# Kernel tuning notes

Hardware: AMD Instinct MI355X
Metric: run time of the kernel (lower is better)

## Reference

```python
import jax, jax.numpy as jnp
import numpy as np

B, T, H, K = 64, 512, 768, 11
START_ID, END_ID = 9, 10  # tag_to_ix['<CLS>'], tag_to_ix['<SEP>']
NEG = -10000.0


def setup_inputs() -> dict:
    key = jax.random.key(0)
    k1, k2, k3, k4 = jax.random.split(key, 4)
    embeds = jax.random.normal(k1, (B, T, H), dtype=jnp.float32)
    W_fc = jax.random.normal(k2, (K, H), dtype=jnp.float32) * 0.02
    b_fc = jax.random.normal(k3, (K,), dtype=jnp.float32) * 0.02
    transitions = jax.random.normal(k4, (K, K), dtype=jnp.float32)
    # __init__ masking: no transition out of anything into START row, none into END col
    transitions = transitions.at[START_ID, :].set(NEG)
    transitions = transitions.at[:, END_ID].set(NEG)
    return {"embeds": embeds, "W_fc": W_fc, "b_fc": b_fc, "transitions": transitions}


def reference(embeds, W_fc, b_fc, transitions):
    # fc projection: feats[b,t,k] (PLM_crf path: encoder output -> Linear)
    feats = jnp.einsum('bth,kh->btk', embeds, W_fc) + b_fc  # [B,T,K]
    Bv, Tv, Kv = feats.shape

    # Viterbi: log_delta init -10000 except start tag; NOTE the original never
    # adds feats[:, 0] (loop starts at t=1), so we faithfully skip it too.
    log_delta0 = jnp.full((Bv, Kv), NEG, dtype=feats.dtype).at[:, START_ID].set(0.0)

    def step(log_delta, feat_t):
        # transitions[i, j]: score of moving from prev tag j to tag i
        scores = transitions[None, :, :] + log_delta[:, None, :]  # [B,K,K]
        psi_t = jnp.argmax(scores, axis=-1)                       # [B,K] best prev tag
        log_delta_new = jnp.max(scores, axis=-1) + feat_t         # [B,K]
        return log_delta_new, psi_t

    feats_seq = jnp.swapaxes(feats[:, 1:], 0, 1)                  # [T-1,B,K]
    log_delta, psi = jax.lax.scan(step, log_delta0, feats_seq)    # psi: [T-1,B,K]

    score = jnp.max(log_delta, axis=-1)                           # [B]
    last_tag = jnp.argmax(log_delta, axis=-1)                     # [B]

    # Backtrack: path[t] = psi[t+1][path[t+1]] for t = T-2 .. 0
    def back(next_tag, psi_t):
        tag = jnp.take_along_axis(psi_t, next_tag[:, None], axis=-1)[:, 0]
        return tag, tag

    _, path_rest = jax.lax.scan(back, last_tag, psi, reverse=True)  # [T-1,B]
    path = jnp.concatenate([jnp.swapaxes(path_rest, 0, 1), last_tag[:, None]], axis=1)  # [B,T]
    return score, path
```

## Files before the change

### kernel.cpp

```cpp
#include <hip/hip_runtime.h>

#define BB 64
#define TT 512
#define HH 768
#define KK 11
#define START_ID 9
#define NEGV -10000.0f
#define ROR1 0x121

typedef float vf2 __attribute__((ext_vector_type(2)));

__device__ __forceinline__ float ror1f(float x) {
    return __int_as_float(__builtin_amdgcn_update_dpp(0, __float_as_int(x), ROR1, 0xF, 0xF, false));
}
__device__ __forceinline__ int ror1i(int x) {
    return __builtin_amdgcn_update_dpp(0, x, ROR1, 0xF, 0xF, false);
}

__device__ __forceinline__ float rlane(float v, int l) {
    return __int_as_float(__builtin_amdgcn_readlane(__float_as_int(v), l));
}

template <int CTRL>
__device__ __forceinline__ float dpp_add(float x) {
    int yi = __builtin_amdgcn_update_dpp(0, __float_as_int(x), CTRL, 0xF, 0xF, false);
    return x + __int_as_float(yi);
}
__device__ __forceinline__ float wave_sum_to_lane63(float x) {
    x = dpp_add<0x111>(x);
    x = dpp_add<0x112>(x);
    x = dpp_add<0x114>(x);
    x = dpp_add<0x118>(x);
    x = dpp_add<0x142>(x);
    x = dpp_add<0x143>(x);
    return x;
}

__global__ __launch_bounds__(256) void fc_kernel(const float* __restrict__ embeds,
                                                 const float* __restrict__ W,
                                                 const float* __restrict__ bias,
                                                 float* __restrict__ feats) {
    const int lane = threadIdx.x & 63;
    const int wave_id = (blockIdx.x * blockDim.x + threadIdx.x) >> 6;

    float4 wf[KK][3];
#pragma unroll
    for (int k = 0; k < KK; ++k)
#pragma unroll
        for (int r = 0; r < 3; ++r)
            wf[k][r] = *reinterpret_cast<const float4*>(W + k * HH + r * 256 + lane * 4);

    float bk[KK];
#pragma unroll
    for (int k = 0; k < KK; ++k) bk[k] = bias[k];

    const int base = wave_id * 8;
#pragma unroll 1
    for (int rr = 0; rr < 8; rr += 2) {
        const float* ea = embeds + (size_t)(base + rr) * HH;
        const float* eb = ea + HH;
        float4 a0 = *reinterpret_cast<const float4*>(ea + 0   + lane * 4);
        float4 a1 = *reinterpret_cast<const float4*>(ea + 256 + lane * 4);
        float4 a2 = *reinterpret_cast<const float4*>(ea + 512 + lane * 4);
        float4 b0 = *reinterpret_cast<const float4*>(eb + 0   + lane * 4);
        float4 b1 = *reinterpret_cast<const float4*>(eb + 256 + lane * 4);
        float4 b2 = *reinterpret_cast<const float4*>(eb + 512 + lane * 4);

        vf2 va[6] = {{a0.x, a0.y}, {a0.z, a0.w}, {a1.x, a1.y},
                     {a1.z, a1.w}, {a2.x, a2.y}, {a2.z, a2.w}};
        vf2 vb[6] = {{b0.x, b0.y}, {b0.z, b0.w}, {b1.x, b1.y},
                     {b1.z, b1.w}, {b2.x, b2.y}, {b2.z, b2.w}};

        float rA[KK], rB[KK];
#pragma unroll
        for (int k = 0; k < KK; ++k) {
            vf2 wv0 = {wf[k][0].x, wf[k][0].y}, wv1 = {wf[k][0].z, wf[k][0].w};
            vf2 wv2 = {wf[k][1].x, wf[k][1].y}, wv3 = {wf[k][1].z, wf[k][1].w};
            vf2 wv4 = {wf[k][2].x, wf[k][2].y}, wv5 = {wf[k][2].z, wf[k][2].w};
            vf2 sA = va[0] * wv0;
            vf2 sB = vb[0] * wv0;
            sA += va[1] * wv1;  sB += vb[1] * wv1;
            sA += va[2] * wv2;  sB += vb[2] * wv2;
            sA += va[3] * wv3;  sB += vb[3] * wv3;
            sA += va[4] * wv4;  sB += vb[4] * wv4;
            sA += va[5] * wv5;  sB += vb[5] * wv5;
            rA[k] = wave_sum_to_lane63(sA.x + sA.y);
            rB[k] = wave_sum_to_lane63(sB.x + sB.y);
        }
        if (lane == 63) {
            float* oA = feats + (size_t)(base + rr) * KK;
#pragma unroll
            for (int k = 0; k < KK; ++k) oA[k] = rA[k] + bk[k];
#pragma unroll
            for (int k = 0; k < KK; ++k) oA[KK + k] = rB[k] + bk[k];
        }
    }
}

__global__ __launch_bounds__(256) void viterbi_kernel(const float* __restrict__ feats,
                                                      const float* __restrict__ trans,
                                                      float* __restrict__ out) {
    __shared__ __align__(16) float feats_lds[(TT + 4) * KK];
    __shared__ __align__(16) float dh[(TT - 1) * 12];
    __shared__ int psi_lds[(TT - 1) * KK];
    __shared__ float tr_lds[KK * KK];
    __shared__ int comp[15 * KK];
    __shared__ int bt[16];
    __shared__ int sh_last;

    const int tid = threadIdx.x;
    const int b = blockIdx.x;

    {
        const float4* src = reinterpret_cast<const float4*>(feats + (size_t)b * TT * KK);
        float4* dst = reinterpret_cast<float4*>(feats_lds);
        for (int i = tid; i < TT * KK / 4; i += 256) dst[i] = src[i];
        if (tid < KK * KK) tr_lds[tid] = trans[tid];
    }
    __syncthreads();

    if (tid < 64) {
        const int i = tid & 15;
        const int g = tid >> 4;
        const bool real = (i < KK);
        const int ci = real ? i : 0;

        int jr[16];
        {
            int jx = i;
#pragma unroll
            for (int r = 0; r < 16; ++r) { jr[r] = jx; jx = ror1i(jx); }
        }
        float trr[16];
#pragma unroll
        for (int r = 0; r < 16; ++r)
            trr[r] = (real && jr[r] < KK) ? tr_lds[i * KK + jr[r]] : NEGV;

        float delta = (i == START_ID) ? 0.0f : NEGV;

        auto vstep = [&](int t, float fcur) {
            if (g == 0 && real) dh[(t - 1) * 12 + i] = delta;
            float cur = delta;
            float acc = trr[0] + cur;
#pragma unroll
            for (int r = 1; r < 16; ++r) {
                cur = ror1f(cur);
                acc = fmaxf(acc, trr[r] + cur);
            }
            delta = acc + fcur;
        };

        float fr0 = feats_lds[1 * KK + ci];
        float fr1 = feats_lds[2 * KK + ci];
        float fr2 = feats_lds[3 * KK + ci];
        float fr3 = feats_lds[4 * KK + ci];

        int t = 1;
#pragma unroll 1
        for (; t <= TT - 4; t += 4) {
            vstep(t,     fr0); fr0 = feats_lds[(t + 4) * KK + ci];
            vstep(t + 1, fr1); fr1 = feats_lds[(t + 5) * KK + ci];
            vstep(t + 2, fr2); fr2 = feats_lds[(t + 6) * KK + ci];
            vstep(t + 3, fr3); fr3 = feats_lds[(t + 7) * KK + ci];
        }
        vstep(TT - 3, fr0);
        vstep(TT - 2, fr1);
        vstep(TT - 1, fr2);

        float dfin[KK];
#pragma unroll
        for (int j = 0; j < KK; ++j) dfin[j] = rlane(delta, j);
        float best = dfin[0];
        int last = 0;
#pragma unroll
        for (int j = 1; j < KK; ++j) {
            bool c = dfin[j] > best;
            best = c ? dfin[j] : best;
            last = c ? j : last;
        }
        if (tid == 0) {
            out[b] = best;
            out[BB + (size_t)b * TT + (TT - 1)] = (float)last;
            sh_last = last;
        }
    }
    __syncthreads();

    {
        const int i = tid & 15;
        const int sg = tid >> 4;
        if (i < KK) {
            float tri[KK];
#pragma unroll
            for (int j = 0; j < KK; ++j) tri[j] = tr_lds[i * KK + j];
            for (int s = sg; s < TT - 1; s += 16) {
                const float4* dr = reinterpret_cast<const float4*>(dh + s * 12);
                float4 a = dr[0], c4 = dr[1], d4 = dr[2];
                float sc[KK] = {tri[0] + a.x,  tri[1] + a.y,  tri[2] + a.z,  tri[3] + a.w,
                                tri[4] + c4.x, tri[5] + c4.y, tri[6] + c4.z, tri[7] + c4.w,
                                tri[8] + d4.x, tri[9] + d4.y, tri[10] + d4.z};
                float bv = sc[0];
                int bj = 0;
#pragma unroll
                for (int j = 1; j < KK; ++j) {
                    bool c = sc[j] > bv;
                    bv = c ? sc[j] : bv;
                    bj = c ? j : bj;
                }
                psi_lds[s * KK + i] = bj;
            }
        }
    }
    __syncthreads();

    {
        const int c = tid >> 4;
        const int i = tid & 15;
        if (c < 15 && i < KK) {
            int cur = i;
            for (int s = c * 32 + 31; s >= c * 32; --s) cur = psi_lds[s * KK + cur];
            comp[c * KK + i] = cur;
        } else if (c == 15 && i == 0) {
            int cur = sh_last;
            float* po = out + BB + (size_t)b * TT;
            for (int s = TT - 2; s >= 480; --s) {
                cur = psi_lds[s * KK + cur];
                po[s] = (float)cur;
            }
            bt[15] = cur;
        }
    }
    __syncthreads();

    if (tid == 0) {
        for (int c = 14; c >= 1; --c) bt[c] = comp[c * KK + bt[c + 1]];
    }
    __syncthreads();

    if (tid < 15) {
        const int c = tid;
        int cur = bt[c + 1];
        float* po = out + BB + (size_t)b * TT;
        for (int s = c * 32 + 31; s >= c * 32; --s) {
            cur = psi_lds[s * KK + cur];
            po[s] = (float)cur;
        }
    }
}

extern "C" void kernel_launch(void* const* d_in, const int* in_sizes, int n_in,
                              void* d_out, int out_size, void* d_ws, size_t ws_size,
                              hipStream_t stream) {
    const float* embeds = (const float*)d_in[0];
    const float* W_fc   = (const float*)d_in[1];
    const float* b_fc   = (const float*)d_in[2];
    const float* trans  = (const float*)d_in[3];
    float* out = (float*)d_out;
    float* feats = (float*)d_ws;

    fc_kernel<<<1024, 256, 0, stream>>>(embeds, W_fc, b_fc, feats);
    viterbi_kernel<<<BB, 256, 0, stream>>>(feats, trans, out);
}
```

Before: 240.0 us.

## Process two sequences per block using readlane broadcasts in Viterbi recurrence

The Viterbi kernel now handles two batch sequences per block, with each 16-lane group of the wave tracking a different sequence. The DPP rotate-based max over previous tags is replaced by broadcasting each previous delta with readlane and doing a tree max. The intent is to halve the block count and shorten the dependency chain through the max. The cost is many scalar readlane operations per step and backtracking both sequences one after the other in each block.

```diff
diff --git a/kernel.cpp b/kernel.cpp
--- a/kernel.cpp
+++ b/kernel.cpp
@@ -6,16 +6,8 @@
 #define KK 11
 #define START_ID 9
 #define NEGV -10000.0f
-#define ROR1 0x121
 
 typedef float vf2 __attribute__((ext_vector_type(2)));
-
-__device__ __forceinline__ float ror1f(float x) {
-    return __int_as_float(__builtin_amdgcn_update_dpp(0, __float_as_int(x), ROR1, 0xF, 0xF, false));
-}
-__device__ __forceinline__ int ror1i(int x) {
-    return __builtin_amdgcn_update_dpp(0, x, ROR1, 0xF, 0xF, false);
-}
 
 __device__ __forceinline__ float rlane(float v, int l) {
     return __int_as_float(__builtin_amdgcn_readlane(__float_as_int(v), l));
@@ -100,93 +92,118 @@
 __global__ __launch_bounds__(256) void viterbi_kernel(const float* __restrict__ feats,
                                                       const float* __restrict__ trans,
                                                       float* __restrict__ out) {
-    __shared__ __align__(16) float feats_lds[(TT + 4) * KK];
-    __shared__ __align__(16) float dh[(TT - 1) * 12];
-    __shared__ int psi_lds[(TT - 1) * KK];
+    __shared__ __align__(16) float feats_lds[2][(TT + 4) * KK];
+    __shared__ __align__(16) float dh[2][(TT - 1) * 12];
+    __shared__ int psi_lds[2][(TT - 1) * KK];
     __shared__ float tr_lds[KK * KK];
     __shared__ int comp[15 * KK];
-    __shared__ int bt[16];
-    __shared__ int sh_last;
+    __shared__ int btb[16];
+    __shared__ int sh_last[2];
 
     const int tid = threadIdx.x;
-    const int b = blockIdx.x;
+    const int b0 = blockIdx.x * 2;
 
     {
-        const float4* src = reinterpret_cast<const float4*>(feats + (size_t)b * TT * KK);
-        float4* dst = reinterpret_cast<float4*>(feats_lds);
-        for (int i = tid; i < TT * KK / 4; i += 256) dst[i] = src[i];
+        const float4* s0 = reinterpret_cast<const float4*>(feats + (size_t)b0 * TT * KK);
+        const float4* s1 = reinterpret_cast<const float4*>(feats + (size_t)(b0 + 1) * TT * KK);
+        float4* d0 = reinterpret_cast<float4*>(&feats_lds[0][0]);
+        float4* d1 = reinterpret_cast<float4*>(&feats_lds[1][0]);
+        for (int i = tid; i < TT * KK / 4; i += 256) { d0[i] = s0[i]; d1[i] = s1[i]; }
         if (tid < KK * KK) tr_lds[tid] = trans[tid];
     }
     __syncthreads();
 
     if (tid < 64) {
-        const int i = tid & 15;
-        const int g = tid >> 4;
+        const int lane = tid;
+        const int i = lane & 15;
+        const int q = (lane >> 4) & 1;
         const bool real = (i < KK);
         const int ci = real ? i : 0;
 
-        int jr[16];
-        {
-            int jx = i;
-#pragma unroll
-            for (int r = 0; r < 16; ++r) { jr[r] = jx; jx = ror1i(jx); }
-        }
-        float trr[16];
-#pragma unroll
-        for (int r = 0; r < 16; ++r)
-            trr[r] = (real && jr[r] < KK) ? tr_lds[i * KK + jr[r]] : NEGV;
-
+        float trr[KK];
+#pragma unroll
+        for (int j = 0; j < KK; ++j) trr[j] = real ? tr_lds[i * KK + j] : NEGV;
+
+        const float* fl = &feats_lds[q][0];
         float delta = (i == START_ID) ? 0.0f : NEGV;
 
         auto vstep = [&](int t, float fcur) {
-            if (g == 0 && real) dh[(t - 1) * 12 + i] = delta;
-            float cur = delta;
-            float acc = trr[0] + cur;
-#pragma unroll
-            for (int r = 1; r < 16; ++r) {
-                cur = ror1f(cur);
-                acc = fmaxf(acc, trr[r] + cur);
-            }
-            delta = acc + fcur;
+            if (lane < 32 && real) dh[q][(t - 1) * 12 + i] = delta;
+            float djA[KK], djB[KK];
+#pragma unroll
+            for (int j = 0; j < KK; ++j) {
+                djA[j] = rlane(delta, j);
+                djB[j] = rlane(delta, 16 + j);
+            }
+            float sA[KK], sB[KK];
+#pragma unroll
+            for (int j = 0; j < KK; ++j) { sA[j] = trr[j] + djA[j]; sB[j] = trr[j] + djB[j]; }
+            float a0 = fmaxf(fmaxf(sA[0], sA[1]), sA[2]);
+            float a1 = fmaxf(fmaxf(sA[3], sA[4]), sA[5]);
+            float a2 = fmaxf(fmaxf(sA[6], sA[7]), sA[8]);
+            float a3 = fmaxf(sA[9], sA[10]);
+            float bestA = fmaxf(fmaxf(fmaxf(a0, a1), a2), a3);
+            float c0 = fmaxf(fmaxf(sB[0], sB[1]), sB[2]);
+            float c1 = fmaxf(fmaxf(sB[3], sB[4]), sB[5]);
+            float c2 = fmaxf(fmaxf(sB[6], sB[7]), sB[8]);
+            float c3 = fmaxf(sB[9], sB[10]);
+            float bestB = fmaxf(fmaxf(fmaxf(c0, c1), c2), c3);
+            float best = q ? bestB : bestA;
+            delta = best + fcur;
         };
 
-        float fr0 = feats_lds[1 * KK + ci];
-        float fr1 = feats_lds[2 * KK + ci];
-        float fr2 = feats_lds[3 * KK + ci];
-        float fr3 = feats_lds[4 * KK + ci];
+        float fr0 = fl[1 * KK + ci];
+        float fr1 = fl[2 * KK + ci];
+        float fr2 = fl[3 * KK + ci];
+        float fr3 = fl[4 * KK + ci];
 
         int t = 1;
 #pragma unroll 1
         for (; t <= TT - 4; t += 4) {
-            vstep(t,     fr0); fr0 = feats_lds[(t + 4) * KK + ci];
-            vstep(t + 1, fr1); fr1 = feats_lds[(t + 5) * KK + ci];
-            vstep(t + 2, fr2); fr2 = feats_lds[(t + 6) * KK + ci];
-            vstep(t + 3, fr3); fr3 = feats_lds[(t + 7) * KK + ci];
+            vstep(t,     fr0); fr0 = fl[(t + 4) * KK + ci];
+            vstep(t + 1, fr1); fr1 = fl[(t + 5) * KK + ci];
+            vstep(t + 2, fr2); fr2 = fl[(t + 6) * KK + ci];
+            vstep(t + 3, fr3); fr3 = fl[(t + 7) * KK + ci];
         }
         vstep(TT - 3, fr0);
         vstep(TT - 2, fr1);
         vstep(TT - 1, fr2);
 
-        float dfin[KK];
-#pragma unroll
-        for (int j = 0; j < KK; ++j) dfin[j] = rlane(delta, j);
-        float best = dfin[0];
-        int last = 0;
-#pragma unroll
-        for (int j = 1; j < KK; ++j) {
-            bool c = dfin[j] > best;
-            best = c ? dfin[j] : best;
-            last = c ? j : last;
+        float dfA[KK], dfB[KK];
+#pragma unroll
+        for (int j = 0; j < KK; ++j) {
+            dfA[j] = rlane(delta, j);
+            dfB[j] = rlane(delta, 16 + j);
         }
         if (tid == 0) {
-            out[b] = best;
-            out[BB + (size_t)b * TT + (TT - 1)] = (float)last;
-            sh_last = last;
+            float best = dfA[0]; int last = 0;
+#pragma unroll
+            for (int j = 1; j < KK; ++j) {
+                bool c = dfA[j] > best;
+                best = c ? dfA[j] : best;
+                last = c ? j : last;
+            }
+            out[b0] = best;
+            out[BB + (size_t)b0 * TT + (TT - 1)] = (float)last;
+            sh_last[0] = last;
+        }
+        if (tid == 1) {
+            float best = dfB[0]; int last = 0;
+#pragma unroll
+            for (int j = 1; j < KK; ++j) {
+                bool c = dfB[j] > best;
+                best = c ? dfB[j] : best;
+                last = c ? j : last;
+            }
+            out[b0 + 1] = best;
+            out[BB + (size_t)(b0 + 1) * TT + (TT - 1)] = (float)last;
+            sh_last[1] = last;
         }
     }
     __syncthreads();
 
-    {
+#pragma unroll 1
+    for (int q = 0; q < 2; ++q) {
         const int i = tid & 15;
         const int sg = tid >> 4;
         if (i < KK) {
@@ -194,7 +211,7 @@
 #pragma unroll
             for (int j = 0; j < KK; ++j) tri[j] = tr_lds[i * KK + j];
             for (int s = sg; s < TT - 1; s += 16) {
-                const float4* dr = reinterpret_cast<const float4*>(dh + s * 12);
+                const float4* dr = reinterpret_cast<const float4*>(&dh[q][s * 12]);
                 float4 a = dr[0], c4 = dr[1], d4 = dr[2];
                 float sc[KK] = {tri[0] + a.x,  tri[1] + a.y,  tri[2] + a.z,  tri[3] + a.w,
                                 tri[4] + c4.x, tri[5] + c4.y, tri[6] + c4.z, tri[7] + c4.w,
@@ -207,44 +224,48 @@
                     bv = c ? sc[j] : bv;
                     bj = c ? j : bj;
                 }
-                psi_lds[s * KK + i] = bj;
+                psi_lds[q][s * KK + i] = bj;
             }
         }
     }
     __syncthreads();
 
-    {
-        const int c = tid >> 4;
-        const int i = tid & 15;
-        if (c < 15 && i < KK) {
-            int cur = i;
-            for (int s = c * 32 + 31; s >= c * 32; --s) cur = psi_lds[s * KK + cur];
-            comp[c * KK + i] = cur;
-        } else if (c == 15 && i == 0) {
-            int cur = sh_last;
-            float* po = out + BB + (size_t)b * TT;
-            for (int s = TT - 2; s >= 480; --s) {
-                cur = psi_lds[s * KK + cur];
+#pragma unroll 1
+    for (int q = 0; q < 2; ++q) {
+        {
+            const int c = tid >> 4;
+            const int i = tid & 15;
+            if (c < 15 && i < KK) {
+                int cur = i;
+                for (int s = c * 32 + 31; s >= c * 32; --s) cur = psi_lds[q][s * KK + cur];
+                comp[c * KK + i] = cur;
+            } else if (c == 15 && i == 0) {
+                int cur = sh_last[q];
+                float* po = out + BB + (size_t)(b0 + q) * TT;
+                for (int s = TT - 2; s >= 480; --s) {
+                    cur = psi_lds[q][s * KK + cur];
+                    po[s] = (float)cur;
+                }
+                btb[15] = cur;
+            }
+        }
+        __syncthreads();
+
+        if (tid == 0) {
+            for (int c = 14; c >= 1; --c) btb[c] = comp[c * KK + btb[c + 1]];
+        }
+        __syncthreads();
+
+        if (tid < 15) {
+            const int c = tid;
+            int cur = btb[c + 1];
+            float* po = out + BB + (size_t)(b0 + q) * TT;
+            for (int s = c * 32 + 31; s >= c * 32; --s) {
+                cur = psi_lds[q][s * KK + cur];
                 po[s] = (float)cur;
             }
-            bt[15] = cur;
-        }
-    }
-    __syncthreads();
-
-    if (tid == 0) {
-        for (int c = 14; c >= 1; --c) bt[c] = comp[c * KK + bt[c + 1]];
-    }
-    __syncthreads();
-
-    if (tid < 15) {
-        const int c = tid;
-        int cur = bt[c + 1];
-        float* po = out + BB + (size_t)b * TT;
-        for (int s = c * 32 + 31; s >= c * 32; --s) {
-            cur = psi_lds[s * KK + cur];
-            po[s] = (float)cur;
-        }
+        }
+        __syncthreads();
     }
 }
 
@@ -259,5 +280,5 @@
     float* feats = (float*)d_ws;
 
     fc_kernel<<<1024, 256, 0, stream>>>(embeds, W_fc, b_fc, feats);
-    viterbi_kernel<<<BB, 256, 0, stream>>>(feats, trans, out);
-}
+    viterbi_kernel<<<32, 256, 0, stream>>>(feats, trans, out);
+}
```

Measured after the change: 238.6 us. No clear change (-0.6%).
